# Kernel optimization log

Hardware: AMD Instinct MI355X
Metric: run time of the kernel (lower is better)

## Reference

```python
import jax, jax.numpy as jnp
import numpy as np

N_SLICES, H, W = 64, 64, 64
VD, VH, VW = 64, 64, 64
K = 3            # PSF kernel size per axis
RES = 1.5        # res_s / res_r
GAP = 1.0        # through-plane slice spacing in recon voxels
N_ITER = 2       # CG iterations (init kwarg)


def _rotmat(ax, ay, az):
    cx, sx = np.cos(ax), np.sin(ax)
    cy, sy = np.cos(ay), np.sin(ay)
    cz, sz = np.cos(az), np.sin(az)
    Rx = np.array([[1, 0, 0], [0, cx, -sx], [0, sx, cx]])
    Ry = np.array([[cy, 0, sy], [0, 1, 0], [-sy, 0, cy]])
    Rz = np.array([[cz, -sz, 0], [sz, cz, 0], [0, 0, 1]])
    return Rz @ Ry @ Rx


def setup_inputs() -> dict:
    rng = np.random.default_rng(0)
    R = np.stack([_rotmat(*rng.normal(0.0, 0.05, 3)) for _ in range(N_SLICES)])
    t = np.zeros((N_SLICES, 3))
    t[:, :2] = rng.normal(0.0, 1.0, (N_SLICES, 2))
    t[:, 2] = (np.arange(N_SLICES) - (N_SLICES - 1) / 2) * GAP + rng.normal(0.0, 0.3, N_SLICES)
    transforms = jnp.asarray(np.concatenate([R, t[:, :, None]], -1), jnp.float32)  # (S,3,4)
    k1, k2 = jax.random.split(jax.random.key(0))
    slices = jax.random.uniform(k1, (N_SLICES, H, W), jnp.float32)
    volume = jax.random.uniform(k2, (VD, VH, VW), jnp.float32) * 0.1
    g = np.arange(K) - (K - 1) / 2
    gz, gy, gx = np.meshgrid(g, g, g, indexing='ij')
    psf = np.exp(-(gx ** 2 + gy ** 2) / (2 * 0.6 ** 2) - gz ** 2 / (2 * 1.0 ** 2))
    psf = jnp.asarray(psf / psf.sum(), jnp.float32)
    return {"transforms": transforms, "slices": slices, "volume": volume, "psf": psf}


def _positions(transforms):
    # PSF sample positions of every slice pixel, mapped into volume voxel coords (xyz).
    xs = (jnp.arange(W) - (W - 1) / 2) * RES
    ys = (jnp.arange(H) - (H - 1) / 2) * RES
    o = jnp.arange(K) - (K - 1) / 2
    oz, oy, ox = jnp.meshgrid(o, o, o, indexing='ij')
    off = jnp.stack([ox, oy, oz], -1).reshape(-1, 3)              # (K^3, 3)
    base = jnp.stack(jnp.broadcast_arrays(xs[None, :], ys[:, None], jnp.zeros((H, W))), -1)
    pts = base[None] + off[:, None, None, :]                      # (K^3, H, W, 3) slice frame
    R, tr = transforms[:, :, :3], transforms[:, :, 3]
    pos = jnp.einsum('sij,khwj->skhwi', R, pts) + tr[:, None, None, None, :]
    center = jnp.array([(VW - 1) / 2, (VH - 1) / 2, (VD - 1) / 2], jnp.float32)
    return pos + center                                           # (S, K^3, H, W, 3)


def _corner_iter(pos):
    # yields the 8 trilinear corners: (clipped int indices (z,y,x), weight with OOB zeroed)
    x, y, z = pos[..., 0], pos[..., 1], pos[..., 2]
    x0, y0, z0 = jnp.floor(x), jnp.floor(y), jnp.floor(z)
    fx, fy, fz = x - x0, y - y0, z - z0
    for dz in (0, 1):
        for dy in (0, 1):
            for dx in (0, 1):
                xi, yi, zi = x0 + dx, y0 + dy, z0 + dz
                w = (fx if dx else 1 - fx) * (fy if dy else 1 - fy) * (fz if dz else 1 - fz)
                valid = (xi >= 0) & (xi < VW) & (yi >= 0) & (yi < VH) & (zi >= 0) & (zi < VD)
                w = jnp.where(valid, w, 0.0)
                yield (jnp.clip(zi, 0, VD - 1).astype(jnp.int32),
                       jnp.clip(yi, 0, VH - 1).astype(jnp.int32),
                       jnp.clip(xi, 0, VW - 1).astype(jnp.int32)), w


def _A(vol, pos, psf_flat):
    # slice_acquisition: trilinear gather + PSF-weighted sum -> (S,H,W)
    acc = jnp.zeros(pos.shape[:-1], vol.dtype)
    for (zi, yi, xi), w in _corner_iter(pos):
        acc = acc + w * vol[zi, yi, xi]
    return jnp.einsum('k,skhw->shw', psf_flat, acc)


def _At(slc, pos, psf_flat):
    # slice_acquisition_adjoint: PSF-weighted trilinear scatter-add -> (VD,VH,VW)
    vals = psf_flat[None, :, None, None] * slc[:, None]           # (S,K^3,H,W)
    vol = jnp.zeros((VD, VH, VW), slc.dtype)
    for (zi, yi, xi), w in _corner_iter(pos):
        vol = vol.at[zi, yi, xi].add(w * vals)
    return vol


def _cg(Afun, b, x0, n_iter):
    x = x0
    r = b - Afun(x)
    p = r
    rr = jnp.vdot(r, r)
    for i in range(n_iter):
        Ap = Afun(p)
        alpha = rr / jnp.vdot(p, Ap)
        x = x + alpha * p
        if i == n_iter - 1:
            break
        r = r - alpha * Ap
        rr_new = jnp.vdot(r, r)
        p = r + (rr_new / rr) * p
        rr = rr_new
    return x


def reference(transforms, slices, volume, psf):
    pos = _positions(transforms)
    psf_flat = psf.reshape(-1)
    AtA = lambda v: _At(_A(v, pos, psf_flat), pos, psf_flat)
    b = _At(slices, pos, psf_flat)
    x = _cg(AtA, b, volume, N_ITER)
    return jax.nn.relu(x)
```

## Files before the change

### kernel.cpp

```cpp
#include <hip/hip_runtime.h>

#define NS 64
#define HH 64
#define WW 64
#define VD 64
#define VH 64
#define VW 64
#define NVOX (VD*VH*VW)
#define NPIX (NS*HH*WW)
#define RES 1.5f
#define NTAB (NS*27)
#define WIN 6
#define SPLIT 8
#define COL_PAD 67
#define GP_ROW 68
#define GP_SLC (66*GP_ROW)
#define GP_TOT (NS*GP_SLC)
#define BAND 16

__global__ __launch_bounds__(256) void k_setup(const float* __restrict__ tr,
                                               const float* __restrict__ psf,
                                               float* __restrict__ tab) {
    int i = blockIdx.x * 256 + threadIdx.x;
    if (i >= NTAB) return;
    int s = i / 27, k = i % 27;
    const float* p = tr + s * 12;
    float R00 = p[0], R01 = p[1], R02 = p[2],  t0 = p[3];
    float R10 = p[4], R11 = p[5], R12 = p[6],  t1 = p[7];
    float R20 = p[8], R21 = p[9], R22 = p[10], t2 = p[11];
    float Ux = RES * R00, Uy = RES * R10, Uz = RES * R20;
    float Vx = RES * R01, Vy = RES * R11, Vz = RES * R21;
    float ox = (float)(k % 3 - 1), oy = (float)((k / 3) % 3 - 1), oz = (float)(k / 9 - 1);
    float Cx = t0 + 31.5f + R00 * ox + R01 * oy + R02 * oz - 31.5f * (Ux + Vx);
    float Cy = t1 + 31.5f + R10 * ox + R11 * oy + R12 * oz - 31.5f * (Uy + Vy);
    float Cz = t2 + 31.5f + R20 * ox + R21 * oy + R22 * oz - 31.5f * (Uz + Vz);
    float inv = 1.f / (Ux * Vy - Uy * Vx);
    float* e = tab + i * 16;
    e[0] = Vy * inv;  e[1] = -Uy * inv;  e[2] = -Vx * inv; e[3] = Ux * inv;
    e[4] = Ux; e[5] = Uy; e[6] = Vx; e[7] = Vy;
    e[8] = Uz; e[9] = Vz; e[10] = Cx; e[11] = Cy;
    e[12] = Cz; e[13] = psf[k]; e[14] = 0.f; e[15] = 0.f;
}

__device__ __forceinline__ float trilin_gather_bf(const float* __restrict__ vol,
                                                  float px, float py, float pz) {
    float x0 = floorf(px), y0 = floorf(py), z0 = floorf(pz);
    float fx = px - x0, fy = py - y0, fz = pz - z0;
    int ix = (int)x0, iy = (int)y0, iz = (int)z0;

    float wx0 = ((unsigned)ix       < 64u) ? (1.f - fx) : 0.f;
    float wx1 = ((unsigned)(ix + 1) < 64u) ? fx         : 0.f;
    float wy0 = ((unsigned)iy       < 64u) ? (1.f - fy) : 0.f;
    float wy1 = ((unsigned)(iy + 1) < 64u) ? fy         : 0.f;
    float wz0 = ((unsigned)iz       < 64u) ? (1.f - fz) : 0.f;
    float wz1 = ((unsigned)(iz + 1) < 64u) ? fz         : 0.f;

    int xc0 = min(max(ix, 0), 63),     xc1 = min(max(ix + 1, 0), 63);
    int yc0 = min(max(iy, 0), 63) << 6,  yc1 = min(max(iy + 1, 0), 63) << 6;
    int zc0 = min(max(iz, 0), 63) << 12, zc1 = min(max(iz + 1, 0), 63) << 12;

    float v000 = vol[zc0 + yc0 + xc0], v001 = vol[zc0 + yc0 + xc1];
    float v010 = vol[zc0 + yc1 + xc0], v011 = vol[zc0 + yc1 + xc1];
    float v100 = vol[zc1 + yc0 + xc0], v101 = vol[zc1 + yc0 + xc1];
    float v110 = vol[zc1 + yc1 + xc0], v111 = vol[zc1 + yc1 + xc1];

    float w00 = wx0 * wy0, w01 = wx1 * wy0, w10 = wx0 * wy1, w11 = wx1 * wy1;
    float lo = fmaf(w00, v000, fmaf(w01, v001, fmaf(w10, v010, w11 * v011)));
    float hi = fmaf(w00, v100, fmaf(w01, v101, fmaf(w10, v110, w11 * v111)));
    return fmaf(wz0, lo, wz1 * hi);
}

template<bool SUB>
__global__ __launch_bounds__(256) void k_a(const float* __restrict__ vin,
                                           float* __restrict__ gp,
                                           const float* __restrict__ tr,
                                           const float* __restrict__ psf,
                                           const float* __restrict__ slc) {
    __shared__ float s_psf[27];
    if (threadIdx.x < 27) s_psf[threadIdx.x] = psf[threadIdx.x];
    __syncthreads();
    int gid = blockIdx.x * 256 + threadIdx.x;
    int s = gid >> 12;
    int h = (gid >> 6) & 63, w = gid & 63;
    const float* p = tr + s * 12;
    float R0 = p[0], R1 = p[1], R2 = p[2],  t0 = p[3];
    float R3 = p[4], R4 = p[5], R5 = p[6],  t1 = p[7];
    float R6 = p[8], R7 = p[9], R8 = p[10], t2 = p[11];
    float xs = ((float)w - 31.5f) * RES;
    float ys = ((float)h - 31.5f) * RES;
    float p0x = fmaf(R0, xs, fmaf(R1, ys, t0)) + 31.5f;
    float p0y = fmaf(R3, xs, fmaf(R4, ys, t1)) + 31.5f;
    float p0z = fmaf(R6, xs, fmaf(R7, ys, t2)) + 31.5f;
    float a = 0.f;
#pragma unroll
    for (int k = 0; k < 27; ++k) {
        const float ox = (float)(k % 3 - 1), oy = (float)((k / 3) % 3 - 1), oz = (float)(k / 9 - 1);
        float px = p0x + ox * R0 + oy * R1 + oz * R2;
        float py = p0y + ox * R3 + oy * R4 + oz * R5;
        float pz = p0z + ox * R6 + oy * R7 + oz * R8;
        bool inb = (px > -1.f) & (px < 64.f) & (py > -1.f) & (py < 64.f)
                 & (pz > -1.f) & (pz < 64.f);
        if (inb) a = fmaf(s_psf[k], trilin_gather_bf(vin, px, py, pz), a);
    }
    float outv = SUB ? (slc[gid] - a) : a;
    gp[s * GP_SLC + (h + 1) * GP_ROW + (w + 1)] = outv;
}

__device__ __forceinline__ void bred256(float v, float* dst) {
#pragma unroll
    for (int off = 32; off > 0; off >>= 1) v += __shfl_down(v, off, 64);
    __shared__ float s_red[4];
    int lane = threadIdx.x & 63, wid = threadIdx.x >> 6;
    if (lane == 0) s_red[wid] = v;
    __syncthreads();
    if (threadIdx.x == 0) atomicAdd(dst, s_red[0] + s_red[1] + s_red[2] + s_red[3]);
}

__device__ __forceinline__ void bred2(float a, float b, float* da, float* db) {
#pragma unroll
    for (int off = 32; off > 0; off >>= 1) {
        a += __shfl_down(a, off, 64);
        b += __shfl_down(b, off, 64);
    }
    __shared__ float s_red[8];
    int lane = threadIdx.x & 63, wid = threadIdx.x >> 6;
    if (lane == 0) { s_red[wid] = a; s_red[4 + wid] = b; }
    __syncthreads();
    if (threadIdx.x == 0) {
        atomicAdd(da, (s_red[0] + s_red[1]) + (s_red[2] + s_red[3]));
        atomicAdd(db, (s_red[4] + s_red[5]) + (s_red[6] + s_red[7]));
    }
}

__global__ __launch_bounds__(512, 2) void k_atv(const float* __restrict__ g,
                                                float* __restrict__ part,
                                                const float* __restrict__ tab) {
    __shared__ float cols[64][COL_PAD];
    __shared__ float sgb[8][BAND * GP_ROW];
    int tid = threadIdx.x;
    {
        float4* c4 = (float4*)&cols[0][0];
#pragma unroll
        for (int i = 0; i < 3; ++i) {
            int j = tid + i * 512;
            if (j < 1072) c4[j] = make_float4(0.f, 0.f, 0.f, 0.f);
        }
    }

    int Yb    = blockIdx.x >> 3;
    int split = blockIdx.x & 7;
    int lane  = tid & 63;
    int wave  = tid >> 6;
    int s = __builtin_amdgcn_readfirstlane(split * 8 + wave);
    float X = (float)lane, Y = (float)Yb;

    const float* tb = tab + s * 27 * 16;

    float hlo = 1e9f, hhi = -1e9f;
    if (lane < 27) {
        const float* e = tb + lane * 16;
        float c = e[1], d = e[3], Cx = e[10], Cy = e[11];
        float ryd = d * (Y - Cy);
        float hs0 = c * (0.f  - Cx) + ryd;
        float hs1 = c * (63.f - Cx) + ryd;
        hlo = fminf(hs0, hs1);
        hhi = fmaxf(hs0, hs1);
    }
#pragma unroll
    for (int off = 32; off > 0; off >>= 1) {
        hlo = fminf(hlo, __shfl_xor(hlo, off, 64));
        hhi = fmaxf(hhi, __shfl_xor(hhi, off, 64));
    }
    int rlo = (int)__builtin_amdgcn_fmed3f(floorf(hlo), -1.f, 63.f) + 1;
    int hbase = min(rlo, 66 - BAND);

    {
        const float4* gs4 = (const float4*)(g + s * GP_SLC + hbase * GP_ROW);
        float4* sd4 = (float4*)&sgb[wave][0];
#pragma unroll
        for (int i = 0; i < 5; ++i) {
            int j = lane + i * 64;
            if (j < 272) sd4[j] = gs4[j];
        }
    }
    __syncthreads();

    const float* ec = tb + 13 * 16;
    float4 ce0 = *(const float4*)(ec);
    float4 ce2 = *(const float4*)(ec + 8);
    float4 ce3 = *(const float4*)(ec + 12);
    float rxc = X - ce2.z, ryc = Y - ce2.w;
    float wsc = ce0.x * rxc + ce0.z * ryc;
    float hsc = ce0.y * rxc + ce0.w * ryc;
    float pzc = fmaf(wsc, ce2.x, fmaf(hsc, ce2.y, ce3.x));
    float basef = floorf(pzc) - 2.f;
    int   basei = (int)basef;

    float acc[WIN];
#pragma unroll
    for (int j = 0; j < WIN; ++j) acc[j] = 0.f;

#pragma unroll 3
    for (int k = 0; k < 27; ++k) {
        const float* e = tb + k * 16;
        float4 e0 = *(const float4*)(e);
        float4 e1 = *(const float4*)(e + 4);
        float4 e2 = *(const float4*)(e + 8);
        float4 e3 = *(const float4*)(e + 12);
        float rx = X - e2.z, ry = Y - e2.w;
        float ws = e0.x * rx + e0.z * ry;
        float hs = e0.y * rx + e0.w * ry;
        float w0f = __builtin_amdgcn_fmed3f(floorf(ws), -1.f, 63.f);
        float h0f = __builtin_amdgcn_fmed3f(floorf(hs), -1.f, 63.f);
        int wA = (int)w0f, hA = (int)h0f;
        float Ux = e1.x, Uy = e1.y, Vx = e1.z, Vy = e1.w;
        float Uz = e2.x, Vz = e2.y;
        float Czb = e3.x - basef;
        float psfk = e3.y;
        float Cxr = -rx, Cyr = -ry;
        int hrel = hA + 1 - hbase;
        int colb = wA + 1;
#pragma unroll
        for (int dh = 0; dh < 2; ++dh) {
            float fh = h0f + (float)dh;
            float tx  = fmaf(fh, Vx, Cxr);
            float ty  = fmaf(fh, Vy, Cyr);
            float tzb = fmaf(fh, Vz, Czb);
            int rowoff = (hrel + dh) * GP_ROW + colb;
#pragma unroll
            for (int dw = 0; dw < 2; ++dw) {
                float fw = w0f + (float)dw;
                float ddx = fmaf(fw, Ux, tx);
                float ddy = fmaf(fw, Uy, ty);
                float wx = fmaxf(1.f - fabsf(ddx), 0.f);
                float wy = fmaxf(1.f - fabsf(ddy), 0.f);
                float gv = sgb[wave][rowoff + dw];
                float val = wx * wy * psfk * gv;
                float prel = fmaf(fw, Uz, tzb);
#pragma unroll
                for (int j = 0; j < WIN; ++j) {
                    float t = fmaxf(0.f, 1.f - fabsf(prel - (float)j));
                    acc[j] = fmaf(val, t, acc[j]);
                }
            }
        }
    }

#pragma unroll
    for (int j = 0; j < WIN; ++j) {
        int zj = basei + j;
        int okz = ((unsigned)zj < 64u);
        int zc = min(max(zj, 0), 63);
        atomicAdd(&cols[lane][zc], okz ? acc[j] : 0.f);
    }
    __syncthreads();

    float* pout = part + split * NVOX + (Yb << 6);
#pragma unroll
    for (int i = 0; i < 8; ++i) {
        int j = tid + i * 512;
        int z = j >> 6, x = j & 63;
        pout[(z << 12) + x] = cols[x][z];
    }
}


__device__ __forceinline__ float sum8(const float* __restrict__ part, int i) {
    float a = 0.f;
#pragma unroll
    for (int j = 0; j < SPLIT; ++j) a += part[j * NVOX + i];
    return a;
}

__global__ __launch_bounds__(256) void k_r0(const float* __restrict__ part,
                                            float* __restrict__ r0,
                                            float* __restrict__ scal) {
    int i = blockIdx.x * 256 + threadIdx.x;
    float rv = sum8(part, i);
    r0[i] = rv;
    bred256(rv * rv, &scal[0]);
}

__global__ __launch_bounds__(256) void k_k1(const float* __restrict__ part,
                                            const float* __restrict__ r0,
                                            float* __restrict__ K1,
                                            float* __restrict__ scal) {
    int i = blockIdx.x * 256 + threadIdx.x;
    float apv = sum8(part, i);
    K1[i] = apv;
    bred2(r0[i] * apv, apv * apv, &scal[1], &scal[2]);
}

__global__ __launch_bounds__(256) void k_dots2(const float* __restrict__ part,
                                               const float* __restrict__ r0,
                                               const float* __restrict__ K1,
                                               float* __restrict__ scal) {
    int i = blockIdx.x * 256 + threadIdx.x;
    float apv = sum8(part, i);
    bred2(r0[i] * apv, K1[i] * apv, &scal[3], &scal[4]);
}

__global__ __launch_bounds__(256) void k_out(const float* __restrict__ x0,
                                             const float* __restrict__ r0,
                                             const float* __restrict__ K1,
                                             const float* __restrict__ scal,
                                             float* __restrict__ out) {
    int i = blockIdx.x * 256 + threadIdx.x;
    float rr0  = scal[0], rK1 = scal[1], K1K1 = scal[2];
    float rK2  = scal[3], K1K2 = scal[4];
    float a0   = rr0 / rK1;
    float rr1  = rr0 - 2.f * a0 * rK1 + a0 * a0 * K1K1;
    float beta = rr1 / rr0;
    float ob   = 1.f + beta;
    float pAp1 = ob * ob * rK1 - ob * a0 * rK2 - a0 * ob * K1K1 + a0 * a0 * K1K2;
    float a1   = rr1 / pAp1;
    float c1   = a0 + a1 * ob;
    float c2   = -a1 * a0;
    float v = fmaf(c2, K1[i], fmaf(c1, r0[i], x0[i]));
    out[i] = v > 0.f ? v : 0.f;
}

extern "C" void kernel_launch(void* const* d_in, const int* in_sizes, int n_in,
                              void* d_out, int out_size, void* d_ws, size_t ws_size,
                              hipStream_t stream) {
    const float* transforms = (const float*)d_in[0];
    const float* slices     = (const float*)d_in[1];
    const float* volume     = (const float*)d_in[2];
    const float* psf        = (const float*)d_in[3];
    float* out = (float*)d_out;

    float* tab    = (float*)d_ws;
    float* gbuf   = tab    + NTAB * 16;
    float* scal   = gbuf   + GP_TOT;
    float* part   = scal   + 8;
    float* r0     = part   + SPLIT * NVOX;
    float* K1     = r0     + NVOX;

    const int ablk = 64 * SPLIT;
    const int fblk = NPIX / 256;
    const int vblk = NVOX / 256;

    hipMemsetAsync(gbuf, 0, (GP_TOT + 8) * sizeof(float), stream);
    k_setup<<<(NTAB + 255) / 256, 256, 0, stream>>>(transforms, psf, tab);

    k_a<true><<<fblk, 256, 0, stream>>>(volume, gbuf, transforms, psf, slices);
    k_atv<<<ablk, 512, 0, stream>>>(gbuf, part, tab);
    k_r0<<<vblk, 256, 0, stream>>>(part, r0, scal);

    k_a<false><<<fblk, 256, 0, stream>>>(r0, gbuf, transforms, psf, nullptr);
    k_atv<<<ablk, 512, 0, stream>>>(gbuf, part, tab);
    k_k1<<<vblk, 256, 0, stream>>>(part, r0, K1, scal);

    k_a<false><<<fblk, 256, 0, stream>>>(K1, gbuf, transforms, psf, nullptr);
    k_atv<<<ablk, 512, 0, stream>>>(gbuf, part, tab);
    k_dots2<<<vblk, 256, 0, stream>>>(part, r0, K1, scal);

    k_out<<<vblk, 256, 0, stream>>>(volume, r0, K1, scal, out);
}
```

Baseline: 293.5 us.

## Fuse memset and setup into first projection kernel; read gradient directly from global

Merges the memset, table setup and first forward projection into a single k_pre launch. Its extra blocks zero only the padded border of the slice buffer and the scalar accumulators, which removes a memset and a kernel launch. Separately, k_atv no longer stages a band of the slice buffer into LDS with a per-wave bounding computation. It gathers the four bilinear neighbours straight from global memory (L1/L2), which frees LDS for occupancy but relies on cache hits for the scattered reads.

```diff
diff --git a/kernel.cpp b/kernel.cpp
--- a/kernel.cpp
+++ b/kernel.cpp
@@ -16,13 +16,10 @@
 #define GP_ROW 68
 #define GP_SLC (66*GP_ROW)
 #define GP_TOT (NS*GP_SLC)
-#define BAND 16
-
-__global__ __launch_bounds__(256) void k_setup(const float* __restrict__ tr,
-                                               const float* __restrict__ psf,
-                                               float* __restrict__ tab) {
-    int i = blockIdx.x * 256 + threadIdx.x;
-    if (i >= NTAB) return;
+
+__device__ __forceinline__ void setup_entry(int i, const float* __restrict__ tr,
+                                            const float* __restrict__ psf,
+                                            float* __restrict__ tab) {
     int s = i / 27, k = i % 27;
     const float* p = tr + s * 12;
     float R00 = p[0], R01 = p[1], R02 = p[2],  t0 = p[3];
@@ -71,15 +68,12 @@
 }
 
 template<bool SUB>
-__global__ __launch_bounds__(256) void k_a(const float* __restrict__ vin,
-                                           float* __restrict__ gp,
-                                           const float* __restrict__ tr,
-                                           const float* __restrict__ psf,
-                                           const float* __restrict__ slc) {
-    __shared__ float s_psf[27];
-    if (threadIdx.x < 27) s_psf[threadIdx.x] = psf[threadIdx.x];
-    __syncthreads();
-    int gid = blockIdx.x * 256 + threadIdx.x;
+__device__ __forceinline__ void a_body(const float* __restrict__ vin,
+                                       float* __restrict__ gp,
+                                       const float* __restrict__ tr,
+                                       const float* __restrict__ s_psf,
+                                       const float* __restrict__ slc,
+                                       int gid) {
     int s = gid >> 12;
     int h = (gid >> 6) & 63, w = gid & 63;
     const float* p = tr + s * 12;
@@ -106,6 +100,45 @@
     gp[s * GP_SLC + (h + 1) * GP_ROW + (w + 1)] = outv;
 }
 
+__global__ __launch_bounds__(256) void k_a(const float* __restrict__ vin,
+                                           float* __restrict__ gp,
+                                           const float* __restrict__ tr,
+                                           const float* __restrict__ psf) {
+    __shared__ float s_psf[27];
+    if (threadIdx.x < 27) s_psf[threadIdx.x] = psf[threadIdx.x];
+    __syncthreads();
+    a_body<false>(vin, gp, tr, s_psf, nullptr, blockIdx.x * 256 + threadIdx.x);
+}
+
+__global__ __launch_bounds__(256) void k_pre(const float* __restrict__ vin,
+                                             float* __restrict__ gp,
+                                             const float* __restrict__ tr,
+                                             const float* __restrict__ psf,
+                                             const float* __restrict__ slc,
+                                             float* __restrict__ tab,
+                                             float* __restrict__ scal) {
+    int b = blockIdx.x;
+    if (b < 1024) {
+        __shared__ float s_psf[27];
+        if (threadIdx.x < 27) s_psf[threadIdx.x] = psf[threadIdx.x];
+        __syncthreads();
+        a_body<true>(vin, gp, tr, s_psf, slc, b * 256 + threadIdx.x);
+    } else if (b < 1032) {
+        int i = (b - 1024) * 256 + threadIdx.x;
+        if (i < NTAB) setup_entry(i, tr, psf, tab);
+    } else {
+        int t = (b - 1032) * 256 + threadIdx.x;
+        for (int j = t; j < GP_TOT; j += 32 * 256) {
+            int rem = j % GP_SLC;
+            int row = rem / GP_ROW;
+            int col = rem - row * GP_ROW;
+            bool border = (row == 0) | (row == 65) | (col == 0) | (col >= 65);
+            if (border) gp[j] = 0.f;
+        }
+        if (t < 8) scal[t] = 0.f;
+    }
+}
+
 __device__ __forceinline__ void bred256(float v, float* dst) {
 #pragma unroll
     for (int off = 32; off > 0; off >>= 1) v += __shfl_down(v, off, 64);
@@ -136,7 +169,6 @@
                                                 float* __restrict__ part,
                                                 const float* __restrict__ tab) {
     __shared__ float cols[64][COL_PAD];
-    __shared__ float sgb[8][BAND * GP_ROW];
     int tid = threadIdx.x;
     {
         float4* c4 = (float4*)&cols[0][0];
@@ -146,6 +178,7 @@
             if (j < 1072) c4[j] = make_float4(0.f, 0.f, 0.f, 0.f);
         }
     }
+    __syncthreads();
 
     int Yb    = blockIdx.x >> 3;
     int split = blockIdx.x & 7;
@@ -155,35 +188,7 @@
     float X = (float)lane, Y = (float)Yb;
 
     const float* tb = tab + s * 27 * 16;
-
-    float hlo = 1e9f, hhi = -1e9f;
-    if (lane < 27) {
-        const float* e = tb + lane * 16;
-        float c = e[1], d = e[3], Cx = e[10], Cy = e[11];
-        float ryd = d * (Y - Cy);
-        float hs0 = c * (0.f  - Cx) + ryd;
-        float hs1 = c * (63.f - Cx) + ryd;
-        hlo = fminf(hs0, hs1);
-        hhi = fmaxf(hs0, hs1);
-    }
-#pragma unroll
-    for (int off = 32; off > 0; off >>= 1) {
-        hlo = fminf(hlo, __shfl_xor(hlo, off, 64));
-        hhi = fmaxf(hhi, __shfl_xor(hhi, off, 64));
-    }
-    int rlo = (int)__builtin_amdgcn_fmed3f(floorf(hlo), -1.f, 63.f) + 1;
-    int hbase = min(rlo, 66 - BAND);
-
-    {
-        const float4* gs4 = (const float4*)(g + s * GP_SLC + hbase * GP_ROW);
-        float4* sd4 = (float4*)&sgb[wave][0];
-#pragma unroll
-        for (int i = 0; i < 5; ++i) {
-            int j = lane + i * 64;
-            if (j < 272) sd4[j] = gs4[j];
-        }
-    }
-    __syncthreads();
+    int gbase = s * GP_SLC;
 
     const float* ec = tb + 13 * 16;
     float4 ce0 = *(const float4*)(ec);
@@ -218,15 +223,14 @@
         float Czb = e3.x - basef;
         float psfk = e3.y;
         float Cxr = -rx, Cyr = -ry;
-        int hrel = hA + 1 - hbase;
-        int colb = wA + 1;
+        int colbase = gbase + wA + 1;
 #pragma unroll
         for (int dh = 0; dh < 2; ++dh) {
             float fh = h0f + (float)dh;
             float tx  = fmaf(fh, Vx, Cxr);
             float ty  = fmaf(fh, Vy, Cyr);
             float tzb = fmaf(fh, Vz, Czb);
-            int rowoff = (hrel + dh) * GP_ROW + colb;
+            int rowoff = colbase + (hA + 1 + dh) * GP_ROW;
 #pragma unroll
             for (int dw = 0; dw < 2; ++dw) {
                 float fw = w0f + (float)dw;
@@ -234,7 +238,7 @@
                 float ddy = fmaf(fw, Uy, ty);
                 float wx = fmaxf(1.f - fabsf(ddx), 0.f);
                 float wy = fmaxf(1.f - fabsf(ddy), 0.f);
-                float gv = sgb[wave][rowoff + dw];
+                float gv = g[rowoff + dw];
                 float val = wx * wy * psfk * gv;
                 float prel = fmaf(fw, Uz, tzb);
 #pragma unroll
@@ -340,18 +344,16 @@
     const int fblk = NPIX / 256;
     const int vblk = NVOX / 256;
 
-    hipMemsetAsync(gbuf, 0, (GP_TOT + 8) * sizeof(float), stream);
-    k_setup<<<(NTAB + 255) / 256, 256, 0, stream>>>(transforms, psf, tab);
-
-    k_a<true><<<fblk, 256, 0, stream>>>(volume, gbuf, transforms, psf, slices);
+    k_pre<<<fblk + 40, 256, 0, stream>>>(volume, gbuf, transforms, psf,
+                                         slices, tab, scal);
     k_atv<<<ablk, 512, 0, stream>>>(gbuf, part, tab);
     k_r0<<<vblk, 256, 0, stream>>>(part, r0, scal);
 
-    k_a<false><<<fblk, 256, 0, stream>>>(r0, gbuf, transforms, psf, nullptr);
+    k_a<<<fblk, 256, 0, stream>>>(r0, gbuf, transforms, psf);
     k_atv<<<ablk, 512, 0, stream>>>(gbuf, part, tab);
     k_k1<<<vblk, 256, 0, stream>>>(part, r0, K1, scal);
 
-    k_a<false><<<fblk, 256, 0, stream>>>(K1, gbuf, transforms, psf, nullptr);
+    k_a<<<fblk, 256, 0, stream>>>(K1, gbuf, transforms, psf);
     k_atv<<<ablk, 512, 0, stream>>>(gbuf, part, tab);
     k_dots2<<<vblk, 256, 0, stream>>>(part, r0, K1, scal);
 
```

New measurement: 274.0 us. 1.07x faster.
